# Performance work log

Hardware: AMD Instinct MI355X
Metric: run time of the kernel (lower is better)

## Reference

```python
import jax, jax.numpy as jnp
import numpy as np


def setup_inputs() -> dict:
    key = jax.random.key(0)
    k1, k2, k3, k4, k5 = jax.random.split(key, 5)
    B, Tx, Ty, E, D = 8, 256, 256, 256, 256
    return {
        "encoder_out_seq": jax.random.normal(k1, (B, Tx, E), dtype=jnp.float32),
        "decoder_out_seq": jax.random.normal(k2, (B, Ty, D), dtype=jnp.float32),
        "W_a": jax.random.normal(k3, (E, E), dtype=jnp.float32) * 0.05,
        "U_a": jax.random.normal(k4, (D, E), dtype=jnp.float32) * 0.05,
        "V_a": jax.random.normal(k5, (E, 1), dtype=jnp.float32) * 0.05,
    }


def reference(encoder_out_seq, decoder_out_seq, W_a, U_a, V_a):
    # encoder_out_seq: [B, Tx, E], decoder_out_seq: [B, Ty, D]
    # Vectorized Bahdanau additive attention (the K.rnn scan is a fake
    # recurrence: each timestep only uses the per-step decoder input and the
    # constant encoder sequence).
    W_dot_s = jnp.einsum("bxe,ef->bxf", encoder_out_seq, W_a)   # [B, Tx, E]
    U_dot_h = jnp.einsum("byd,de->bye", decoder_out_seq, U_a)   # [B, Ty, E]
    # [B, Ty, Tx, E] broadcast add + tanh, then project with V_a -> [B, Ty, Tx]
    Ws_plus_Uh = jnp.tanh(W_dot_s[:, None, :, :] + U_dot_h[:, :, None, :])
    e = jnp.einsum("byxe,eo->byx", Ws_plus_Uh, V_a)             # [B, Ty, Tx]
    e = jax.nn.softmax(e, axis=-1)                               # softmax over Tx
    # context: weighted sum of encoder states -> [B, Ty, E]
    c = jnp.einsum("byx,bxe->bye", e, encoder_out_seq)
    return (c, e)
```

## Files before the change

### kernel.cpp

```cpp
#include <hip/hip_runtime.h>
#include <cstddef>
#include <stdint.h>

#define NB 8
#define TX 256
#define TY 256
#define NE 256

#define CSC 2.8853900817779268f

__device__ __forceinline__ void gload_lds16(const float* g, float* l) {
    __builtin_amdgcn_global_load_lds(
        (const __attribute__((address_space(1))) void*)g,
        (__attribute__((address_space(3))) void*)l,
        16, 0, 0);
}

__global__ __launch_bounds__(512) void prep_kernel(
    const float* __restrict__ enc, const float* __restrict__ dec,
    const float* __restrict__ Wa, const float* __restrict__ Ua,
    float* __restrict__ ZwT, float* __restrict__ Zu)
{
    const int tx = threadIdx.x;
    const int w  = threadIdx.y;
    const int tid = w * 64 + tx;
    int blk = blockIdx.x;
    const bool isU = blk >= 128;
    if (isU) blk -= 128;
    const int b  = blk >> 4;
    const int r0 = (blk & 15) * 16;

    const int rq = (w & 3) * 4;
    const int eh = (w >> 2) * 128;
    const int cc = eh + tx * 2;

    __shared__ float rowsT[256][16];
    __shared__ float MbL[2][16 * 256];
    __shared__ float tL[16][260];

    const float* M = isU ? Ua : Wa;

    const float* src = (isU ? dec : enc) + ((size_t)b * 256 + r0) * NE;
    #pragma unroll
    for (int j = 0; j < 2; ++j) {
        const int f   = tid + j * 512;
        const int row = f & 15;
        const int kq  = f >> 4;
        const float4 v = ((const float4*)src)[row * 64 + kq];
        rowsT[kq * 4 + 0][row] = v.x;
        rowsT[kq * 4 + 1][row] = v.y;
        rowsT[kq * 4 + 2][row] = v.z;
        rowsT[kq * 4 + 3][row] = v.w;
    }
    gload_lds16(M + tid * 4,        MbL[0] + w * 256);
    gload_lds16(M + 2048 + tid * 4, MbL[0] + 2048 + w * 256);
    __syncthreads();

    float2 a0 = make_float2(0.f, 0.f), a1 = a0, a2 = a0, a3 = a0;

    for (int c = 0; c < 16; ++c) {
        if (c < 15) {
            const float* g = M + (size_t)(c + 1) * 4096;
            float* dst = MbL[(c + 1) & 1];
            gload_lds16(g + tid * 4,        dst + w * 256);
            gload_lds16(g + 2048 + tid * 4, dst + 2048 + w * 256);
        }
        const float* mb = MbL[c & 1] + cc;
        const int kbase = c * 16;
        #pragma unroll 8
        for (int j = 0; j < 16; ++j) {
            const float2 mw = *(const float2*)(mb + j * 256);
            const float4 rv = *(const float4*)&rowsT[kbase + j][rq];
            a0.x = __builtin_fmaf(rv.x, mw.x, a0.x);
            a0.y = __builtin_fmaf(rv.x, mw.y, a0.y);
            a1.x = __builtin_fmaf(rv.y, mw.x, a1.x);
            a1.y = __builtin_fmaf(rv.y, mw.y, a1.y);
            a2.x = __builtin_fmaf(rv.z, mw.x, a2.x);
            a2.y = __builtin_fmaf(rv.z, mw.y, a2.y);
            a3.x = __builtin_fmaf(rv.w, mw.x, a3.x);
            a3.y = __builtin_fmaf(rv.w, mw.y, a3.y);
        }
        __syncthreads();
    }

    a0.x = __builtin_amdgcn_exp2f(a0.x * CSC);
    a0.y = __builtin_amdgcn_exp2f(a0.y * CSC);
    a1.x = __builtin_amdgcn_exp2f(a1.x * CSC);
    a1.y = __builtin_amdgcn_exp2f(a1.y * CSC);
    a2.x = __builtin_amdgcn_exp2f(a2.x * CSC);
    a2.y = __builtin_amdgcn_exp2f(a2.y * CSC);
    a3.x = __builtin_amdgcn_exp2f(a3.x * CSC);
    a3.y = __builtin_amdgcn_exp2f(a3.y * CSC);

    if (isU) {
        const int rbase = r0 + rq;
        *(float2*)(Zu + ((size_t)b * TY + rbase + 0) * NE + cc) = a0;
        *(float2*)(Zu + ((size_t)b * TY + rbase + 1) * NE + cc) = a1;
        *(float2*)(Zu + ((size_t)b * TY + rbase + 2) * NE + cc) = a2;
        *(float2*)(Zu + ((size_t)b * TY + rbase + 3) * NE + cc) = a3;
    } else {
        tL[rq + 0][cc] = a0.x; tL[rq + 0][cc + 1] = a0.y;
        tL[rq + 1][cc] = a1.x; tL[rq + 1][cc + 1] = a1.y;
        tL[rq + 2][cc] = a2.x; tL[rq + 2][cc + 1] = a2.y;
        tL[rq + 3][cc] = a3.x; tL[rq + 3][cc + 1] = a3.y;
        __syncthreads();
        #pragma unroll
        for (int rep = 0; rep < 2; ++rep) {
            const int f   = tid + rep * 512;
            const int e   = f >> 2;
            const int xq4 = (f & 3) * 4;
            float4 o;
            o.x = tL[xq4 + 0][e];
            o.y = tL[xq4 + 1][e];
            o.z = tL[xq4 + 2][e];
            o.w = tL[xq4 + 3][e];
            *(float4*)(ZwT + ((size_t)b * NE + e) * TX + r0 + xq4) = o;
        }
    }
}

__global__ __launch_bounds__(512, 2) void attn_kernel(
    const float* __restrict__ enc, const float* __restrict__ ZwT,
    const float* __restrict__ Zu, const float* __restrict__ Va,
    float* __restrict__ c_out, float* __restrict__ e_out)
{
    const int tx = threadIdx.x;
    const int w  = threadIdx.y;
    const int tid = w * 64 + tx;
    const int b  = blockIdx.x & 7;
    const int y0 = (blockIdx.x >> 3) * 8;
    const int y  = y0 + w;

    __shared__ float4 zuLo[NE];
    __shared__ float4 zuHi[NE];
    __shared__ float  vL[NE];
    __shared__ float4 accL[8][8][64];
    __shared__ float  pLT[8][TX];

    {
        const int e = tid & 255;
        const float* zp = Zu + ((size_t)b * TY + y0) * NE + e;
        if (tid < 256) {
            zuLo[e] = make_float4(zp[0], zp[NE], zp[2 * NE], zp[3 * NE]);
            vL[e] = Va[e];
        } else {
            zuHi[e] = make_float4(zp[4 * NE], zp[5 * NE], zp[6 * NE], zp[7 * NE]);
        }
    }
    __syncthreads();

    const float* wp = ZwT + (size_t)b * NE * TX + (size_t)(w * 32) * TX + tx * 4;
    float4 a0 = make_float4(0.f, 0.f, 0.f, 0.f);
    float4 a1 = a0, a2 = a0, a3 = a0, a4 = a0, a5 = a0, a6 = a0, a7 = a0;

#define SC(A, ZU) \
    A.x = __builtin_fmaf(v, __builtin_amdgcn_rcpf(__builtin_fmaf(zw.x, ZU, 1.f)), A.x); \
    A.y = __builtin_fmaf(v, __builtin_amdgcn_rcpf(__builtin_fmaf(zw.y, ZU, 1.f)), A.y); \
    A.z = __builtin_fmaf(v, __builtin_amdgcn_rcpf(__builtin_fmaf(zw.z, ZU, 1.f)), A.z); \
    A.w = __builtin_fmaf(v, __builtin_amdgcn_rcpf(__builtin_fmaf(zw.w, ZU, 1.f)), A.w);

    #pragma unroll 4
    for (int e = 0; e < 32; ++e) {
        const float4 zw = *(const float4*)(wp + (size_t)e * TX);
        const float4 zl = zuLo[w * 32 + e];
        const float4 zh = zuHi[w * 32 + e];
        const float  v  = vL[w * 32 + e];
        SC(a0, zl.x) SC(a1, zl.y) SC(a2, zl.z) SC(a3, zl.w)
        SC(a4, zh.x) SC(a5, zh.y) SC(a6, zh.z) SC(a7, zh.w)
    }
#undef SC
    accL[w][0][tx] = a0; accL[w][1][tx] = a1;
    accL[w][2][tx] = a2; accL[w][3][tx] = a3;
    accL[w][4][tx] = a4; accL[w][5][tx] = a5;
    accL[w][6][tx] = a6; accL[w][7][tx] = a7;
    __syncthreads();

    float4 s = make_float4(0.f, 0.f, 0.f, 0.f);
    #pragma unroll
    for (int ww = 0; ww < 8; ++ww) {
        const float4 a = accL[ww][w][tx];
        s.x += a.x; s.y += a.y; s.z += a.z; s.w += a.w;
    }
    s.x *= -2.f; s.y *= -2.f; s.z *= -2.f; s.w *= -2.f;

    float m = fmaxf(fmaxf(s.x, s.y), fmaxf(s.z, s.w));
    #pragma unroll
    for (int off = 32; off; off >>= 1) m = fmaxf(m, __shfl_xor(m, off));
    float4 p;
    p.x = __expf(s.x - m);
    p.y = __expf(s.y - m);
    p.z = __expf(s.z - m);
    p.w = __expf(s.w - m);
    float sum = (p.x + p.y) + (p.z + p.w);
    #pragma unroll
    for (int off = 32; off; off >>= 1) sum += __shfl_xor(sum, off);
    const float inv = __builtin_amdgcn_rcpf(sum);
    p.x *= inv; p.y *= inv; p.z *= inv; p.w *= inv;

    *(float4*)(e_out + ((size_t)b * TY + y) * TX + tx * 4) = p;
    *(float4*)&pLT[w][tx * 4] = p;
    __syncthreads();

    const float* ep = enc + (size_t)b * TX * NE + (size_t)(w * 32) * NE + tx * 4;
    float4 c0 = make_float4(0.f, 0.f, 0.f, 0.f);
    float4 c1 = c0, c2 = c0, c3 = c0, c4 = c0, c5 = c0, c6 = c0, c7 = c0;

#define CTXY(CY, RP, EV) \
    CY.x = __builtin_fmaf(RP, EV.x, CY.x); \
    CY.y = __builtin_fmaf(RP, EV.y, CY.y); \
    CY.z = __builtin_fmaf(RP, EV.z, CY.z); \
    CY.w = __builtin_fmaf(RP, EV.w, CY.w);
#define CTXI(COMP, EV) \
    CTXY(c0, rp0.COMP, EV) CTXY(c1, rp1.COMP, EV) CTXY(c2, rp2.COMP, EV) CTXY(c3, rp3.COMP, EV) \
    CTXY(c4, rp4.COMP, EV) CTXY(c5, rp5.COMP, EV) CTXY(c6, rp6.COMP, EV) CTXY(c7, rp7.COMP, EV)

    #pragma unroll 2
    for (int g = 0; g < 8; ++g) {
        const int xg = g * 4;
        const float4 rp0 = *(const float4*)&pLT[0][w * 32 + xg];
        const float4 rp1 = *(const float4*)&pLT[1][w * 32 + xg];
        const float4 rp2 = *(const float4*)&pLT[2][w * 32 + xg];
        const float4 rp3 = *(const float4*)&pLT[3][w * 32 + xg];
        const float4 rp4 = *(const float4*)&pLT[4][w * 32 + xg];
        const float4 rp5 = *(const float4*)&pLT[5][w * 32 + xg];
        const float4 rp6 = *(const float4*)&pLT[6][w * 32 + xg];
        const float4 rp7 = *(const float4*)&pLT[7][w * 32 + xg];
        const float4 ev0 = *(const float4*)(ep + (size_t)(xg + 0) * NE);
        const float4 ev1 = *(const float4*)(ep + (size_t)(xg + 1) * NE);
        const float4 ev2 = *(const float4*)(ep + (size_t)(xg + 2) * NE);
        const float4 ev3 = *(const float4*)(ep + (size_t)(xg + 3) * NE);
        CTXI(x, ev0)
        CTXI(y, ev1)
        CTXI(z, ev2)
        CTXI(w, ev3)
    }
#undef CTXI
#undef CTXY

    __syncthreads();
    accL[w][0][tx] = c0; accL[w][1][tx] = c1;
    accL[w][2][tx] = c2; accL[w][3][tx] = c3;
    accL[w][4][tx] = c4; accL[w][5][tx] = c5;
    accL[w][6][tx] = c6; accL[w][7][tx] = c7;
    __syncthreads();

    float4 cs = make_float4(0.f, 0.f, 0.f, 0.f);
    #pragma unroll
    for (int ww = 0; ww < 8; ++ww) {
        const float4 t = accL[ww][w][tx];
        cs.x += t.x; cs.y += t.y; cs.z += t.z; cs.w += t.w;
    }
    *(float4*)(c_out + ((size_t)b * TY + y) * NE + tx * 4) = cs;
}

extern "C" void kernel_launch(void* const* d_in, const int* in_sizes, int n_in,
                              void* d_out, int out_size, void* d_ws, size_t ws_size,
                              hipStream_t stream) {
    const float* enc = (const float*)d_in[0];
    const float* dec = (const float*)d_in[1];
    const float* Wa  = (const float*)d_in[2];
    const float* Ua  = (const float*)d_in[3];
    const float* Va  = (const float*)d_in[4];

    float* c_out = (float*)d_out;
    float* e_out = (float*)d_out + (size_t)NB * TY * NE;

    float* ZwT = (float*)d_ws;
    float* Zu  = (float*)d_ws + (size_t)NB * NE * TX;

    prep_kernel<<<256, dim3(64, 8), 0, stream>>>(enc, dec, Wa, Ua, ZwT, Zu);
    attn_kernel<<<256, dim3(64, 8), 0, stream>>>(enc, ZwT, Zu, Va, c_out, e_out);
}
```

Before: 41.44 us.

## Fuse prep and attention kernels with per-batch atomic counters

Merges the two launches into one 512-block kernel. The first 256 blocks compute the exp-transformed projections and bump a per-batch counter; the remaining blocks spin on that counter before running the attention and context stages. This removes a kernel launch boundary and lets batches whose prep is done start early, but it adds a memset launch and spin-waiting. It relies on prep blocks being scheduled before the waiting blocks (deadlock risk otherwise), and the fused kernel shares one large shared buffer, which may lower occupancy.

```diff
diff --git a/kernel.cpp b/kernel.cpp
--- a/kernel.cpp
+++ b/kernel.cpp
@@ -16,126 +16,138 @@
         16, 0, 0);
 }
 
-__global__ __launch_bounds__(512) void prep_kernel(
+__global__ __launch_bounds__(512) void fused_kernel(
     const float* __restrict__ enc, const float* __restrict__ dec,
     const float* __restrict__ Wa, const float* __restrict__ Ua,
-    float* __restrict__ ZwT, float* __restrict__ Zu)
+    const float* __restrict__ Va, float* __restrict__ ZwT,
+    float* __restrict__ Zu, unsigned int* __restrict__ cnt,
+    float* __restrict__ c_out, float* __restrict__ e_out)
 {
+    __shared__ __align__(16) char smem[82944];
     const int tx = threadIdx.x;
     const int w  = threadIdx.y;
     const int tid = w * 64 + tx;
     int blk = blockIdx.x;
-    const bool isU = blk >= 128;
-    if (isU) blk -= 128;
-    const int b  = blk >> 4;
-    const int r0 = (blk & 15) * 16;
-
-    const int rq = (w & 3) * 4;
-    const int eh = (w >> 2) * 128;
-    const int cc = eh + tx * 2;
-
-    __shared__ float rowsT[256][16];
-    __shared__ float MbL[2][16 * 256];
-    __shared__ float tL[16][260];
-
-    const float* M = isU ? Ua : Wa;
-
-    const float* src = (isU ? dec : enc) + ((size_t)b * 256 + r0) * NE;
-    #pragma unroll
-    for (int j = 0; j < 2; ++j) {
-        const int f   = tid + j * 512;
-        const int row = f & 15;
-        const int kq  = f >> 4;
-        const float4 v = ((const float4*)src)[row * 64 + kq];
-        rowsT[kq * 4 + 0][row] = v.x;
-        rowsT[kq * 4 + 1][row] = v.y;
-        rowsT[kq * 4 + 2][row] = v.z;
-        rowsT[kq * 4 + 3][row] = v.w;
-    }
-    gload_lds16(M + tid * 4,        MbL[0] + w * 256);
-    gload_lds16(M + 2048 + tid * 4, MbL[0] + 2048 + w * 256);
-    __syncthreads();
-
-    float2 a0 = make_float2(0.f, 0.f), a1 = a0, a2 = a0, a3 = a0;
-
-    for (int c = 0; c < 16; ++c) {
-        if (c < 15) {
-            const float* g = M + (size_t)(c + 1) * 4096;
-            float* dst = MbL[(c + 1) & 1];
-            gload_lds16(g + tid * 4,        dst + w * 256);
-            gload_lds16(g + 2048 + tid * 4, dst + 2048 + w * 256);
-        }
-        const float* mb = MbL[c & 1] + cc;
-        const int kbase = c * 16;
-        #pragma unroll 8
-        for (int j = 0; j < 16; ++j) {
-            const float2 mw = *(const float2*)(mb + j * 256);
-            const float4 rv = *(const float4*)&rowsT[kbase + j][rq];
-            a0.x = __builtin_fmaf(rv.x, mw.x, a0.x);
-            a0.y = __builtin_fmaf(rv.x, mw.y, a0.y);
-            a1.x = __builtin_fmaf(rv.y, mw.x, a1.x);
-            a1.y = __builtin_fmaf(rv.y, mw.y, a1.y);
-            a2.x = __builtin_fmaf(rv.z, mw.x, a2.x);
-            a2.y = __builtin_fmaf(rv.z, mw.y, a2.y);
-            a3.x = __builtin_fmaf(rv.w, mw.x, a3.x);
-            a3.y = __builtin_fmaf(rv.w, mw.y, a3.y);
-        }
+
+    if (blk < 256) {
+        const bool isU = blk >= 128;
+        if (isU) blk -= 128;
+        const int b  = blk >> 4;
+        const int r0 = (blk & 15) * 16;
+
+        const int rq  = (w & 3) * 4;
+        const int ehh = (w >> 2) * 128;
+        const int cc  = ehh + tx * 2;
+
+        float* rowsT = (float*)smem;
+        float* MbL   = rowsT + 4096;
+        float* tL    = MbL + 8192;
+
+        const float* M = isU ? Ua : Wa;
+
+        const float* src = (isU ? dec : enc) + ((size_t)b * 256 + r0) * NE;
+        #pragma unroll
+        for (int j = 0; j < 2; ++j) {
+            const int f   = tid + j * 512;
+            const int row = f & 15;
+            const int kq  = f >> 4;
+            const float4 v = ((const float4*)src)[row * 64 + kq];
+            rowsT[(kq * 4 + 0) * 16 + row] = v.x;
+            rowsT[(kq * 4 + 1) * 16 + row] = v.y;
+            rowsT[(kq * 4 + 2) * 16 + row] = v.z;
+            rowsT[(kq * 4 + 3) * 16 + row] = v.w;
+        }
+        gload_lds16(M + tid * 4,        MbL + w * 256);
+        gload_lds16(M + 2048 + tid * 4, MbL + 2048 + w * 256);
         __syncthreads();
-    }
-
-    a0.x = __builtin_amdgcn_exp2f(a0.x * CSC);
-    a0.y = __builtin_amdgcn_exp2f(a0.y * CSC);
-    a1.x = __builtin_amdgcn_exp2f(a1.x * CSC);
-    a1.y = __builtin_amdgcn_exp2f(a1.y * CSC);
-    a2.x = __builtin_amdgcn_exp2f(a2.x * CSC);
-    a2.y = __builtin_amdgcn_exp2f(a2.y * CSC);
-    a3.x = __builtin_amdgcn_exp2f(a3.x * CSC);
-    a3.y = __builtin_amdgcn_exp2f(a3.y * CSC);
-
-    if (isU) {
-        const int rbase = r0 + rq;
-        *(float2*)(Zu + ((size_t)b * TY + rbase + 0) * NE + cc) = a0;
-        *(float2*)(Zu + ((size_t)b * TY + rbase + 1) * NE + cc) = a1;
-        *(float2*)(Zu + ((size_t)b * TY + rbase + 2) * NE + cc) = a2;
-        *(float2*)(Zu + ((size_t)b * TY + rbase + 3) * NE + cc) = a3;
-    } else {
-        tL[rq + 0][cc] = a0.x; tL[rq + 0][cc + 1] = a0.y;
-        tL[rq + 1][cc] = a1.x; tL[rq + 1][cc + 1] = a1.y;
-        tL[rq + 2][cc] = a2.x; tL[rq + 2][cc + 1] = a2.y;
-        tL[rq + 3][cc] = a3.x; tL[rq + 3][cc + 1] = a3.y;
+
+        float2 a0 = make_float2(0.f, 0.f), a1 = a0, a2 = a0, a3 = a0;
+
+        for (int c = 0; c < 16; ++c) {
+            if (c < 15) {
+                const float* g = M + (size_t)(c + 1) * 4096;
+                float* dst = MbL + ((c + 1) & 1) * 4096;
+                gload_lds16(g + tid * 4,        dst + w * 256);
+                gload_lds16(g + 2048 + tid * 4, dst + 2048 + w * 256);
+            }
+            const float* mb = MbL + (c & 1) * 4096 + cc;
+            const int kbase = c * 16;
+            #pragma unroll 8
+            for (int j = 0; j < 16; ++j) {
+                const float2 mw = *(const float2*)(mb + j * 256);
+                const float4 rv = *(const float4*)&rowsT[(kbase + j) * 16 + rq];
+                a0.x = __builtin_fmaf(rv.x, mw.x, a0.x);
+                a0.y = __builtin_fmaf(rv.x, mw.y, a0.y);
+                a1.x = __builtin_fmaf(rv.y, mw.x, a1.x);
+                a1.y = __builtin_fmaf(rv.y, mw.y, a1.y);
+                a2.x = __builtin_fmaf(rv.z, mw.x, a2.x);
+                a2.y = __builtin_fmaf(rv.z, mw.y, a2.y);
+                a3.x = __builtin_fmaf(rv.w, mw.x, a3.x);
+                a3.y = __builtin_fmaf(rv.w, mw.y, a3.y);
+            }
+            __syncthreads();
+        }
+
+        a0.x = __builtin_amdgcn_exp2f(a0.x * CSC);
+        a0.y = __builtin_amdgcn_exp2f(a0.y * CSC);
+        a1.x = __builtin_amdgcn_exp2f(a1.x * CSC);
+        a1.y = __builtin_amdgcn_exp2f(a1.y * CSC);
+        a2.x = __builtin_amdgcn_exp2f(a2.x * CSC);
+        a2.y = __builtin_amdgcn_exp2f(a2.y * CSC);
+        a3.x = __builtin_amdgcn_exp2f(a3.x * CSC);
+        a3.y = __builtin_amdgcn_exp2f(a3.y * CSC);
+
+        if (isU) {
+            const int rbase = r0 + rq;
+            *(float2*)(Zu + ((size_t)b * TY + rbase + 0) * NE + cc) = a0;
+            *(float2*)(Zu + ((size_t)b * TY + rbase + 1) * NE + cc) = a1;
+            *(float2*)(Zu + ((size_t)b * TY + rbase + 2) * NE + cc) = a2;
+            *(float2*)(Zu + ((size_t)b * TY + rbase + 3) * NE + cc) = a3;
+        } else {
+            tL[(rq + 0) * 260 + cc] = a0.x; tL[(rq + 0) * 260 + cc + 1] = a0.y;
+            tL[(rq + 1) * 260 + cc] = a1.x; tL[(rq + 1) * 260 + cc + 1] = a1.y;
+            tL[(rq + 2) * 260 + cc] = a2.x; tL[(rq + 2) * 260 + cc + 1] = a2.y;
+            tL[(rq + 3) * 260 + cc] = a3.x; tL[(rq + 3) * 260 + cc + 1] = a3.y;
+            __syncthreads();
+            #pragma unroll
+            for (int rep = 0; rep < 2; ++rep) {
+                const int f   = tid + rep * 512;
+                const int e   = f >> 2;
+                const int xq4 = (f & 3) * 4;
+                float4 o;
+                o.x = tL[(xq4 + 0) * 260 + e];
+                o.y = tL[(xq4 + 1) * 260 + e];
+                o.z = tL[(xq4 + 2) * 260 + e];
+                o.w = tL[(xq4 + 3) * 260 + e];
+                *(float4*)(ZwT + ((size_t)b * NE + e) * TX + r0 + xq4) = o;
+            }
+        }
+
         __syncthreads();
-        #pragma unroll
-        for (int rep = 0; rep < 2; ++rep) {
-            const int f   = tid + rep * 512;
-            const int e   = f >> 2;
-            const int xq4 = (f & 3) * 4;
-            float4 o;
-            o.x = tL[xq4 + 0][e];
-            o.y = tL[xq4 + 1][e];
-            o.z = tL[xq4 + 2][e];
-            o.w = tL[xq4 + 3][e];
-            *(float4*)(ZwT + ((size_t)b * NE + e) * TX + r0 + xq4) = o;
-        }
-    }
-}
-
-__global__ __launch_bounds__(512, 2) void attn_kernel(
-    const float* __restrict__ enc, const float* __restrict__ ZwT,
-    const float* __restrict__ Zu, const float* __restrict__ Va,
-    float* __restrict__ c_out, float* __restrict__ e_out)
-{
-    const int tx = threadIdx.x;
-    const int w  = threadIdx.y;
-    const int tid = w * 64 + tx;
-    const int b  = blockIdx.x & 7;
-    const int y0 = (blockIdx.x >> 3) * 8;
+        if (tid == 0)
+            __hip_atomic_fetch_add(&cnt[b], 1u, __ATOMIC_RELEASE,
+                                   __HIP_MEMORY_SCOPE_AGENT);
+        return;
+    }
+
+    blk -= 256;
+    const int b  = blk & 7;
+    const int y0 = (blk >> 3) * 8;
     const int y  = y0 + w;
 
-    __shared__ float4 zuLo[NE];
-    __shared__ float4 zuHi[NE];
-    __shared__ float  vL[NE];
-    __shared__ float4 accL[8][8][64];
-    __shared__ float  pLT[8][TX];
+    if (tid == 0) {
+        while (__hip_atomic_load(&cnt[b], __ATOMIC_ACQUIRE,
+                                 __HIP_MEMORY_SCOPE_AGENT) < 32u)
+            __builtin_amdgcn_s_sleep(8);
+    }
+    __syncthreads();
+
+    float4* zuLo = (float4*)smem;
+    float4* zuHi = (float4*)(smem + 4096);
+    float*  vL   = (float*)(smem + 8192);
+    float4* accL = (float4*)(smem + 9216);
+    float*  pLT  = (float*)(smem + 9216 + 65536);
+#define ACC(W, Y, T) accL[((W) * 8 + (Y)) * 64 + (T)]
 
     {
         const int e = tid & 255;
@@ -169,16 +181,16 @@
         SC(a4, zh.x) SC(a5, zh.y) SC(a6, zh.z) SC(a7, zh.w)
     }
 #undef SC
-    accL[w][0][tx] = a0; accL[w][1][tx] = a1;
-    accL[w][2][tx] = a2; accL[w][3][tx] = a3;
-    accL[w][4][tx] = a4; accL[w][5][tx] = a5;
-    accL[w][6][tx] = a6; accL[w][7][tx] = a7;
+    ACC(w, 0, tx) = a0; ACC(w, 1, tx) = a1;
+    ACC(w, 2, tx) = a2; ACC(w, 3, tx) = a3;
+    ACC(w, 4, tx) = a4; ACC(w, 5, tx) = a5;
+    ACC(w, 6, tx) = a6; ACC(w, 7, tx) = a7;
     __syncthreads();
 
     float4 s = make_float4(0.f, 0.f, 0.f, 0.f);
     #pragma unroll
     for (int ww = 0; ww < 8; ++ww) {
-        const float4 a = accL[ww][w][tx];
+        const float4 a = ACC(ww, w, tx);
         s.x += a.x; s.y += a.y; s.z += a.z; s.w += a.w;
     }
     s.x *= -2.f; s.y *= -2.f; s.z *= -2.f; s.w *= -2.f;
@@ -198,7 +210,7 @@
     p.x *= inv; p.y *= inv; p.z *= inv; p.w *= inv;
 
     *(float4*)(e_out + ((size_t)b * TY + y) * TX + tx * 4) = p;
-    *(float4*)&pLT[w][tx * 4] = p;
+    *(float4*)&pLT[w * 256 + tx * 4] = p;
     __syncthreads();
 
     const float* ep = enc + (size_t)b * TX * NE + (size_t)(w * 32) * NE + tx * 4;
@@ -217,14 +229,14 @@
     #pragma unroll 2
     for (int g = 0; g < 8; ++g) {
         const int xg = g * 4;
-        const float4 rp0 = *(const float4*)&pLT[0][w * 32 + xg];
-        const float4 rp1 = *(const float4*)&pLT[1][w * 32 + xg];
-        const float4 rp2 = *(const float4*)&pLT[2][w * 32 + xg];
-        const float4 rp3 = *(const float4*)&pLT[3][w * 32 + xg];
-        const float4 rp4 = *(const float4*)&pLT[4][w * 32 + xg];
-        const float4 rp5 = *(const float4*)&pLT[5][w * 32 + xg];
-        const float4 rp6 = *(const float4*)&pLT[6][w * 32 + xg];
-        const float4 rp7 = *(const float4*)&pLT[7][w * 32 + xg];
+        const float4 rp0 = *(const float4*)&pLT[0 * 256 + w * 32 + xg];
+        const float4 rp1 = *(const float4*)&pLT[1 * 256 + w * 32 + xg];
+        const float4 rp2 = *(const float4*)&pLT[2 * 256 + w * 32 + xg];
+        const float4 rp3 = *(const float4*)&pLT[3 * 256 + w * 32 + xg];
+        const float4 rp4 = *(const float4*)&pLT[4 * 256 + w * 32 + xg];
+        const float4 rp5 = *(const float4*)&pLT[5 * 256 + w * 32 + xg];
+        const float4 rp6 = *(const float4*)&pLT[6 * 256 + w * 32 + xg];
+        const float4 rp7 = *(const float4*)&pLT[7 * 256 + w * 32 + xg];
         const float4 ev0 = *(const float4*)(ep + (size_t)(xg + 0) * NE);
         const float4 ev1 = *(const float4*)(ep + (size_t)(xg + 1) * NE);
         const float4 ev2 = *(const float4*)(ep + (size_t)(xg + 2) * NE);
@@ -238,19 +250,20 @@
 #undef CTXY
 
     __syncthreads();
-    accL[w][0][tx] = c0; accL[w][1][tx] = c1;
-    accL[w][2][tx] = c2; accL[w][3][tx] = c3;
-    accL[w][4][tx] = c4; accL[w][5][tx] = c5;
-    accL[w][6][tx] = c6; accL[w][7][tx] = c7;
+    ACC(w, 0, tx) = c0; ACC(w, 1, tx) = c1;
+    ACC(w, 2, tx) = c2; ACC(w, 3, tx) = c3;
+    ACC(w, 4, tx) = c4; ACC(w, 5, tx) = c5;
+    ACC(w, 6, tx) = c6; ACC(w, 7, tx) = c7;
     __syncthreads();
 
     float4 cs = make_float4(0.f, 0.f, 0.f, 0.f);
     #pragma unroll
     for (int ww = 0; ww < 8; ++ww) {
-        const float4 t = accL[ww][w][tx];
+        const float4 t = ACC(ww, w, tx);
         cs.x += t.x; cs.y += t.y; cs.z += t.z; cs.w += t.w;
     }
     *(float4*)(c_out + ((size_t)b * TY + y) * NE + tx * 4) = cs;
+#undef ACC
 }
 
 extern "C" void kernel_launch(void* const* d_in, const int* in_sizes, int n_in,
@@ -266,8 +279,10 @@
     float* e_out = (float*)d_out + (size_t)NB * TY * NE;
 
     float* ZwT = (float*)d_ws;
-    float* Zu  = (float*)d_ws + (size_t)NB * NE * TX;
-
-    prep_kernel<<<256, dim3(64, 8), 0, stream>>>(enc, dec, Wa, Ua, ZwT, Zu);
-    attn_kernel<<<256, dim3(64, 8), 0, stream>>>(enc, ZwT, Zu, Va, c_out, e_out);
+    float* Zu  = ZwT + (size_t)NB * NE * TX;
+    unsigned int* cnt = (unsigned int*)(Zu + (size_t)NB * TY * NE);
+
+    hipMemsetAsync(cnt, 0, NB * sizeof(unsigned int), stream);
+    fused_kernel<<<512, dim3(64, 8), 0, stream>>>(
+        enc, dec, Wa, Ua, Va, ZwT, Zu, cnt, c_out, e_out);
 }
```

Measured after the change: 63.19 us. 1.52x slower.
